# Optimization experiments

Hardware: AMD Instinct MI355X
Metric: run time of the kernel (lower is better)

The kernel has to match this reference:

```python
import jax, jax.numpy as jnp
import numpy as np

C = 512        # concept_num
D = 256        # input_dim / embedding_dim
H = 512        # msg_hidden_dim
M = 256        # msg_output_dim
OH = 512       # hidden_dim
T = 2          # edge_type_num
E = C * (C - 1)  # fully-connected graph without self-loops = 261632


def _glorot(key, shape, fan_in):
    return jax.random.normal(key, shape, jnp.float32) / np.sqrt(fan_in).astype(np.float32)


def setup_inputs() -> dict:
    key = jax.random.key(0)
    ks = jax.random.split(key, 12)
    inputs = jax.random.normal(ks[0], (C, D), jnp.float32)
    rel_type = jax.random.uniform(ks[1], (E, T), jnp.float32)
    send_idx = jax.random.randint(ks[2], (E,), 0, C, jnp.int32)
    rec_idx = jax.random.randint(ks[3], (E,), 0, C, jnp.int32)
    # per-edge-type message MLP params, stacked over type dim
    W1 = _glorot(ks[4], (T, 2 * D, H), 2 * D)
    b1 = jnp.zeros((T, H), jnp.float32)
    W2 = _glorot(ks[5], (T, H, M), H)
    b2 = jnp.zeros((T, M), jnp.float32)
    # output MLP params
    Wo1 = _glorot(ks[6], (M, OH), M)
    bo1 = jnp.zeros((OH,), jnp.float32)
    Wo2 = _glorot(ks[7], (OH, OH), OH)
    bo2 = jnp.zeros((OH,), jnp.float32)
    Wo3 = _glorot(ks[8], (OH, D), OH)
    bo3 = jnp.zeros((D,), jnp.float32)
    return {"inputs": inputs, "rel_type": rel_type, "W1": W1, "b1": b1,
            "W2": W2, "b2": b2, "Wo1": Wo1, "bo1": bo1, "Wo2": Wo2,
            "bo2": bo2, "Wo3": Wo3, "bo3": bo3,
            "send_idx": send_idx, "rec_idx": rec_idx}


def reference(inputs, rel_type, W1, b1, W2, b2, Wo1, bo1, Wo2, bo2, Wo3, bo3,
              send_idx, rec_idx):
    # node2edge: one-hot sparse matmul == index gather
    senders = jnp.take(inputs, send_idx, axis=0)      # [E, D]
    receivers = jnp.take(inputs, rec_idx, axis=0)     # [E, D]
    pre_msg = jnp.concatenate([senders, receivers], axis=-1)  # [E, 2D]
    # per-edge-type MLPs, weighted-summed by rel_type (dropout=0 / eval mode)
    all_msgs = jnp.zeros((pre_msg.shape[0], M), jnp.float32)
    for i in range(T):
        msg = jax.nn.relu(pre_msg @ W1[i] + b1[i])    # [E, H]
        msg = jax.nn.relu(msg @ W2[i] + b2[i])        # [E, M]
        all_msgs = all_msgs + msg * rel_type[:, i:i + 1]
    # edge2node: transposed one-hot sparse matmul == scatter-add over receivers
    agg_msgs = jax.ops.segment_sum(all_msgs, rec_idx, num_segments=inputs.shape[0])  # [C, M]
    pred = jax.nn.relu(agg_msgs @ Wo1 + bo1)
    pred = jax.nn.relu(pred @ Wo2 + bo2)
    return pred @ Wo3 + bo3                           # [C, D]
```

## Files before the change

kernel.cpp:

```cpp
#include <hip/hip_runtime.h>

#define C_N   512
#define E_N   261632
#define CAP   768

typedef _Float16 f16;
typedef _Float16 f16x8_t __attribute__((ext_vector_type(8)));
typedef float    f32x16_t __attribute__((ext_vector_type(16)));

__global__ __launch_bounds__(256) void k_prep_all(
    const float* __restrict__ inputs, const float* __restrict__ W1,
    const float* __restrict__ b1, const float* __restrict__ W2,
    const float* __restrict__ Wo1, const float* __restrict__ Wo2, const float* __restrict__ Wo3,
    f16* __restrict__ SA, f16* __restrict__ RB, f16* __restrict__ W2p,
    f16* __restrict__ Wo1p, f16* __restrict__ Wo2p, f16* __restrict__ Wo3p,
    int* __restrict__ cnt, float* __restrict__ agg)
{
  __shared__ f16 wt[2][256][18];
  int bid = blockIdx.x;
  int tid = threadIdx.x;
  if (bid < 64) {
    int lane = tid & 63, w = tid >> 6;
    int hlf = lane >> 5, l31 = lane & 31;
    int br = bid & 7, bc = (bid >> 3) & 1, mi = bid >> 4;
    int t = mi >> 1, half = mi & 1;
    const float* Wsrc = W1 + (size_t)t * 512 * 512 + (size_t)half * 256 * 512;

    f32x16_t acc[2][2];
    #pragma unroll
    for (int rt = 0; rt < 2; rt++)
      #pragma unroll
      for (int ctl = 0; ctl < 2; ctl++)
        #pragma unroll
        for (int r = 0; r < 16; r++) acc[rt][ctl][r] = 0.f;

    #pragma unroll
    for (int i = 0; i < 4; i++) {
      int idx = tid + i * 256;
      int k = idx >> 6, n4 = idx & 63;
      float4 v = *(const float4*)&Wsrc[(size_t)k * 512 + bc * 256 + n4 * 4];
      wt[0][n4 * 4 + 0][k] = (f16)v.x;
      wt[0][n4 * 4 + 1][k] = (f16)v.y;
      wt[0][n4 * 4 + 2][k] = (f16)v.z;
      wt[0][n4 * 4 + 3][k] = (f16)v.w;
    }

    for (int kc = 0; kc < 16; kc++) {
      __syncthreads();
      if (kc + 1 < 16) {
        int b = (kc + 1) & 1;
        #pragma unroll
        for (int i = 0; i < 4; i++) {
          int idx = tid + i * 256;
          int k = idx >> 6, n4 = idx & 63;
          float4 v = *(const float4*)&Wsrc[(size_t)((kc + 1) * 16 + k) * 512 + bc * 256 + n4 * 4];
          wt[b][n4 * 4 + 0][k] = (f16)v.x;
          wt[b][n4 * 4 + 1][k] = (f16)v.y;
          wt[b][n4 * 4 + 2][k] = (f16)v.z;
          wt[b][n4 * 4 + 3][k] = (f16)v.w;
        }
      }
      f16x8_t af[2];
      #pragma unroll
      for (int rt = 0; rt < 2; rt++) {
        const float4* p = (const float4*)&inputs[(size_t)(br * 64 + rt * 32 + l31) * 256 + kc * 16 + hlf * 8];
        float4 u0 = p[0], u1 = p[1];
        af[rt] = (f16x8_t){(f16)u0.x, (f16)u0.y, (f16)u0.z, (f16)u0.w,
                           (f16)u1.x, (f16)u1.y, (f16)u1.z, (f16)u1.w};
      }
      int b = kc & 1;
      #pragma unroll
      for (int ctl = 0; ctl < 2; ctl++) {
        int n = (2 * w + ctl) * 32 + l31;
        f16x8_t bfr = *(const f16x8_t*)&wt[b][n][hlf * 8];
        #pragma unroll
        for (int rt = 0; rt < 2; rt++)
          acc[rt][ctl] = __builtin_amdgcn_mfma_f32_32x32x16_f16(af[rt], bfr, acc[rt][ctl], 0, 0, 0);
      }
    }
    f16* dst = (half == 0) ? SA : RB;
    #pragma unroll
    for (int ctl = 0; ctl < 2; ctl++) {
      int col = bc * 256 + (2 * w + ctl) * 32 + l31;
      float bias = (half == 1) ? b1[t * 512 + col] : 0.f;
      #pragma unroll
      for (int rt = 0; rt < 2; rt++)
        #pragma unroll
        for (int r = 0; r < 16; r++) {
          int row = br * 64 + rt * 32 + (r & 3) + 8 * (r >> 2) + 4 * hlf;
          dst[((size_t)(t * 512 + row)) * 512 + col] = (f16)(acc[rt][ctl][r] + bias);
        }
    }
  } else if (bid < 192) {
    int gid  = (bid - 64) * 256 + tid;
    int lane = gid & 63;
    int ct   = (gid >> 6) & 7;
    int kc   = (gid >> 9) & 31;
    int t    = gid >> 14;
    int n    = ct * 32 + (lane & 31);
    int k0   = kc * 16 + (lane >> 5) * 8;
    const float* src = W2 + (size_t)t * 512 * 256;
    f16x8_t v;
    #pragma unroll
    for (int j = 0; j < 8; j++) v[j] = (f16)src[(size_t)(k0 + j) * 256 + n];
    *(f16x8_t*)(W2p + (size_t)gid * 8) = v;
  } else if (bid < 256) {
    int gid  = (bid - 192) * 256 + tid;
    int lane = gid & 63;
    int ct   = (gid >> 6) & 15;
    int kc   = gid >> 10;
    int n    = ct * 32 + (lane & 31);
    int k0   = kc * 16 + (lane >> 5) * 8;
    f16x8_t v;
    #pragma unroll
    for (int j = 0; j < 8; j++) v[j] = (f16)Wo1[(size_t)(k0 + j) * 512 + n];
    *(f16x8_t*)(Wo1p + (size_t)gid * 8) = v;
  } else if (bid < 384) {
    int gid  = (bid - 256) * 256 + tid;
    int lane = gid & 63;
    int ct   = (gid >> 6) & 15;
    int kc   = gid >> 10;
    int n    = ct * 32 + (lane & 31);
    int k0   = kc * 16 + (lane >> 5) * 8;
    f16x8_t v;
    #pragma unroll
    for (int j = 0; j < 8; j++) v[j] = (f16)Wo2[(size_t)(k0 + j) * 512 + n];
    *(f16x8_t*)(Wo2p + (size_t)gid * 8) = v;
  } else if (bid < 448) {
    int gid  = (bid - 384) * 256 + tid;
    int lane = gid & 63;
    int ct   = (gid >> 6) & 7;
    int kc   = gid >> 9;
    int n    = ct * 32 + (lane & 31);
    int k0   = kc * 16 + (lane >> 5) * 8;
    f16x8_t v;
    #pragma unroll
    for (int j = 0; j < 8; j++) v[j] = (f16)Wo3[(size_t)(k0 + j) * 256 + n];
    *(f16x8_t*)(Wo3p + (size_t)gid * 8) = v;
  } else if (bid == 448) {
    for (int i = tid; i < 512 * 16; i += 256) cnt[i] = 0;
  } else {
    float4* a4 = (float4*)agg;
    for (int i = tid; i < 512 * 64; i += 256) a4[i] = make_float4(0.f, 0.f, 0.f, 0.f);
  }
}

__global__ __launch_bounds__(512) void k_scatter_d(const int* __restrict__ rec,
    const int* __restrict__ send, const float* __restrict__ rel,
    int* __restrict__ cnt, uint2* __restrict__ smeta)
{
  __shared__ int lh[512];
  __shared__ int lb[512];
  int b = blockIdx.x;
  int e0 = b * (E_N / 128);
  lh[threadIdx.x] = 0;
  __syncthreads();
  for (int i = threadIdx.x; i < E_N / 128; i += 512)
    atomicAdd(&lh[rec[e0 + i]], 1);
  __syncthreads();
  {
    int c = lh[threadIdx.x];
    lb[threadIdx.x] = c ? atomicAdd(&cnt[threadIdx.x * 16], c) : 0;
    lh[threadIdx.x] = 0;
  }
  __syncthreads();
  for (int i = threadIdx.x; i < E_N / 128; i += 512) {
    int e = e0 + i;
    int r = rec[e];
    int p = r * CAP + lb[r] + atomicAdd(&lh[r], 1);
    f16 r0 = (f16)rel[2 * (size_t)e];
    f16 r1 = (f16)rel[2 * (size_t)e + 1];
    unsigned pk = ((unsigned)__builtin_bit_cast(unsigned short, r1) << 16)
                |  (unsigned)__builtin_bit_cast(unsigned short, r0);
    smeta[p] = make_uint2((unsigned)send[e], pk);
  }
}

#define H1S 136

__global__ __launch_bounds__(512, 4) void k_edges(
    const f16* __restrict__ SA, const f16* __restrict__ RB,
    const f16* __restrict__ W2p, const float* __restrict__ b2,
    const uint2* __restrict__ smeta, const int* __restrict__ cnt,
    float* __restrict__ agg)
{
  __shared__ f16   h1[2][128][H1S];
  __shared__ f16   rbs[2][512];
  __shared__ float b2s[2][256];
  __shared__ float aggL[2][256];
  __shared__ __align__(16) float relv[2][128];
  __shared__ int   sends[128];

  int c   = blockIdx.x;
  int ti  = blockIdx.y;
  int n_c = cnt[c * 16];
  if (ti * 128 >= n_c) return;

  int tid  = threadIdx.x;
  int lane = tid & 63;
  int w    = tid >> 6;
  int hlf  = lane >> 5;
  int l31  = lane & 31;
  int q4   = tid & 15;
  int rb0  = tid >> 4;
  int rg   = w >> 2;
  int cg   = w & 3;

  if (tid < 128) {
    int t = tid >> 6, qq = tid & 63;
    *(f16x8_t*)&rbs[t][qq * 8] = *(const f16x8_t*)&RB[((size_t)(t * 512 + c)) * 512 + qq * 8];
  }
  ((float*)aggL)[tid] = 0.f;
  { int t = (tid >> 8) & 1, col = tid & 255; b2s[t][col] = b2[t * 256 + col]; }

  int s0 = c * CAP + ti * 128;
  int nv = n_c - ti * 128; if (nv > 128) nv = 128;

  if (tid < 128) {
    if (tid < nv) {
      uint2 m = smeta[s0 + tid];
      sends[tid] = (int)m.x;
      relv[0][tid] = (float)__builtin_bit_cast(f16, (unsigned short)(m.y & 0xffffu));
      relv[1][tid] = (float)__builtin_bit_cast(f16, (unsigned short)(m.y >> 16));
    } else {
      sends[tid] = 0; relv[0][tid] = 0.f; relv[1][tid] = 0.f;
    }
  }
  __syncthreads();

  const f16x8_t* SAc = (const f16x8_t*)SA;
  const f16x8_t* Bp  = (const f16x8_t*)W2p;

  const f16 fz = (f16)0.f;
  const f16x8_t z8 = {fz, fz, fz, fz, fz, fz, fz, fz};

  int voff[4];
  #pragma unroll
  for (int j = 0; j < 4; j++)
    voff[j] = sends[rb0 + 32 * j] * 64 + q4;

  f16x8_t g[4];

  #pragma unroll
  for (int j = 0; j < 4; j++) g[j] = SAc[voff[j]];
  {
    f16x8_t rbq = *(const f16x8_t*)&rbs[0][q4 * 8];
    #pragma unroll
    for (int j = 0; j < 4; j++) {
      f16x8_t sv = g[j] + rbq;
      sv = __builtin_elementwise_max(sv, z8);
      *(f16x8_t*)&h1[0][rb0 + 32 * j][q4 * 8] = sv;
    }
  }

  f32x16_t acc[2][2];

  for (int p = 0; p < 8; p++) {
    int t  = p >> 2;
    int ks = p & 3;
    int pb = p & 1;
    __syncthreads();

    if (p < 7) {
      int off = ((p + 1) >> 2) * 32768 + ((p + 1) & 3) * 16;
      #pragma unroll
      for (int j = 0; j < 4; j++) g[j] = SAc[voff[j] + off];
    }

    if (ks == 0) {
      #pragma unroll
      for (int a = 0; a < 2; a++)
        #pragma unroll
        for (int b_ = 0; b_ < 2; b_++)
          #pragma unroll
          for (int r = 0; r < 16; r++) acc[a][b_][r] = 0.f;
    }

    const f16x8_t* Bw = Bp + ((size_t)((t * 32 + ks * 8) * 8 + cg * 2) * 64 + lane);

    f16x8_t bb[2][2];
    bb[0][0] = Bw[0];    bb[0][1] = Bw[64];
    bb[1][0] = Bw[512];  bb[1][1] = Bw[512 + 64];

    const f16* h1b = &h1[pb][0][0];
    int a0 = (rg * 64 + l31) * H1S + hlf * 8;
    #pragma unroll
    for (int kc = 0; kc < 8; kc++) {
      int qb = kc & 1;
      f16x8_t af0 = *(const f16x8_t*)&h1b[a0 + kc * 16];
      f16x8_t af1 = *(const f16x8_t*)&h1b[a0 + 32 * H1S + kc * 16];
      acc[0][0] = __builtin_amdgcn_mfma_f32_32x32x16_f16(af0, bb[qb][0], acc[0][0], 0, 0, 0);
      acc[0][1] = __builtin_amdgcn_mfma_f32_32x32x16_f16(af0, bb[qb][1], acc[0][1], 0, 0, 0);
      acc[1][0] = __builtin_amdgcn_mfma_f32_32x32x16_f16(af1, bb[qb][0], acc[1][0], 0, 0, 0);
      acc[1][1] = __builtin_amdgcn_mfma_f32_32x32x16_f16(af1, bb[qb][1], acc[1][1], 0, 0, 0);
      if (kc + 2 < 8) {
        bb[qb][0] = Bw[(kc + 2) * 512];
        bb[qb][1] = Bw[(kc + 2) * 512 + 64];
      }
    }

    if (ks == 3) {
      #pragma unroll
      for (int ctl = 0; ctl < 2; ctl++) {
        int col = (cg * 2 + ctl) * 32 + l31;
        float b2c = b2s[t][col];
        float csum = 0.f;
        #pragma unroll
        for (int rt = 0; rt < 2; rt++) {
          int rbase = rg * 64 + rt * 32 + 4 * hlf;
          #pragma unroll
          for (int grp = 0; grp < 4; grp++) {
            float4 rv = *(const float4*)&relv[t][rbase + 8 * grp];
            float v0 = fmaxf(acc[rt][ctl][grp * 4 + 0] + b2c, 0.f);
            float v1 = fmaxf(acc[rt][ctl][grp * 4 + 1] + b2c, 0.f);
            float v2 = fmaxf(acc[rt][ctl][grp * 4 + 2] + b2c, 0.f);
            float v3 = fmaxf(acc[rt][ctl][grp * 4 + 3] + b2c, 0.f);
            csum += v0 * rv.x + v1 * rv.y + v2 * rv.z + v3 * rv.w;
          }
        }
        csum += __shfl_xor(csum, 32, 64);
        if (hlf == 0) aggL[rg][col] += csum;
      }
    }

    if (p < 7) {
      int tn = (p + 1) >> 2, ksn = (p + 1) & 3;
      f16x8_t rbq = *(const f16x8_t*)&rbs[tn][ksn * 128 + q4 * 8];
      #pragma unroll
      for (int j = 0; j < 4; j++) {
        f16x8_t sv = g[j] + rbq;
        sv = __builtin_elementwise_max(sv, z8);
        *(f16x8_t*)&h1[pb ^ 1][rb0 + 32 * j][q4 * 8] = sv;
      }
    }
  }

  __syncthreads();

  if (tid < 256) atomicAdd(&agg[(size_t)c * 256 + tid], aggL[0][tid] + aggL[1][tid]);
}

#define HOS 520

__global__ __launch_bounds__(512, 1) void k_omlp(const float* __restrict__ agg,
    const f16* __restrict__ Wo1p, const float* __restrict__ bo1,
    const f16* __restrict__ Wo2p, const float* __restrict__ bo2,
    const f16* __restrict__ Wo3p, const float* __restrict__ bo3,
    float* __restrict__ out)
{
  __shared__ f16 hL1[32 * HOS];
  __shared__ f16 hL2[32 * HOS];
  int tid = threadIdx.x, lane = tid & 63, w = tid >> 6;
  int hlf = lane >> 5, l31 = lane & 31;
  int br = blockIdx.x;

  {
    f32x16_t acc[2];
    #pragma unroll
    for (int ctl = 0; ctl < 2; ctl++)
      #pragma unroll
      for (int r = 0; r < 16; r++) acc[ctl][r] = 0.f;
    for (int kc = 0; kc < 16; kc++) {
      const float4* p = (const float4*)&agg[(size_t)(br * 32 + l31) * 256 + kc * 16 + hlf * 8];
      float4 u0 = p[0], u1 = p[1];
      f16x8_t af = (f16x8_t){(f16)u0.x, (f16)u0.y, (f16)u0.z, (f16)u0.w,
                             (f16)u1.x, (f16)u1.y, (f16)u1.z, (f16)u1.w};
      #pragma unroll
      for (int ctl = 0; ctl < 2; ctl++) {
        int ct = 2 * w + ctl;
        f16x8_t bfr = *(const f16x8_t*)&Wo1p[((size_t)(kc * 16 + ct) * 64 + lane) * 8];
        acc[ctl] = __builtin_amdgcn_mfma_f32_32x32x16_f16(af, bfr, acc[ctl], 0, 0, 0);
      }
    }
    #pragma unroll
    for (int ctl = 0; ctl < 2; ctl++) {
      int col = (2 * w + ctl) * 32 + l31;
      float bias = bo1[col];
      #pragma unroll
      for (int r = 0; r < 16; r++) {
        int row = (r & 3) + 8 * (r >> 2) + 4 * hlf;
        hL1[row * HOS + col] = (f16)fmaxf(acc[ctl][r] + bias, 0.f);
      }
    }
  }
  __syncthreads();

  {
    f32x16_t acc[2];
    #pragma unroll
    for (int ctl = 0; ctl < 2; ctl++)
      #pragma unroll
      for (int r = 0; r < 16; r++) acc[ctl][r] = 0.f;
    for (int kc = 0; kc < 32; kc++) {
      f16x8_t af = *(const f16x8_t*)&hL1[l31 * HOS + kc * 16 + hlf * 8];
      #pragma unroll
      for (int ctl = 0; ctl < 2; ctl++) {
        int ct = 2 * w + ctl;
        f16x8_t bfr = *(const f16x8_t*)&Wo2p[((size_t)(kc * 16 + ct) * 64 + lane) * 8];
        acc[ctl] = __builtin_amdgcn_mfma_f32_32x32x16_f16(af, bfr, acc[ctl], 0, 0, 0);
      }
    }
    #pragma unroll
    for (int ctl = 0; ctl < 2; ctl++) {
      int col = (2 * w + ctl) * 32 + l31;
      float bias = bo2[col];
      #pragma unroll
      for (int r = 0; r < 16; r++) {
        int row = (r & 3) + 8 * (r >> 2) + 4 * hlf;
        hL2[row * HOS + col] = (f16)fmaxf(acc[ctl][r] + bias, 0.f);
      }
    }
  }
  __syncthreads();

  {
    f32x16_t acc;
    #pragma unroll
    for (int r = 0; r < 16; r++) acc[r] = 0.f;
    for (int kc = 0; kc < 32; kc++) {
      f16x8_t af  = *(const f16x8_t*)&hL2[l31 * HOS + kc * 16 + hlf * 8];
      f16x8_t bfr = *(const f16x8_t*)&Wo3p[((size_t)(kc * 8 + w) * 64 + lane) * 8];
      acc = __builtin_amdgcn_mfma_f32_32x32x16_f16(af, bfr, acc, 0, 0, 0);
    }
    int col = w * 32 + l31;
    float bias = bo3[col];
    #pragma unroll
    for (int r = 0; r < 16; r++) {
      int row = br * 32 + (r & 3) + 8 * (r >> 2) + 4 * hlf;
      out[(size_t)row * 256 + col] = acc[r] + bias;
    }
  }
}

extern "C" void kernel_launch(void* const* d_in, const int* in_sizes, int n_in,
                              void* d_out, int out_size, void* d_ws, size_t ws_size,
                              hipStream_t stream)
{
  (void)in_sizes; (void)n_in; (void)out_size; (void)ws_size;
  const float* inputs = (const float*)d_in[0];
  const float* rel    = (const float*)d_in[1];
  const float* W1     = (const float*)d_in[2];
  const float* b1     = (const float*)d_in[3];
  const float* W2     = (const float*)d_in[4];
  const float* b2     = (const float*)d_in[5];
  const float* Wo1    = (const float*)d_in[6];
  const float* bo1    = (const float*)d_in[7];
  const float* Wo2    = (const float*)d_in[8];
  const float* bo2    = (const float*)d_in[9];
  const float* Wo3    = (const float*)d_in[10];
  const float* bo3    = (const float*)d_in[11];
  const int* send_idx = (const int*)d_in[12];
  const int* rec_idx  = (const int*)d_in[13];
  float* out = (float*)d_out;

  char* ws = (char*)d_ws;
  f16*    SA    = (f16*)   (ws);
  f16*    RB    = (f16*)   (ws + (1024u << 10));
  f16*    W2p   = (f16*)   (ws + (2048u << 10));
  float*  agg   = (float*) (ws + (2560u << 10));
  int*    cnt   = (int*)   (ws + (3072u << 10));
  f16*    Wo1p  = (f16*)   (ws + (3136u << 10));
  f16*    Wo2p  = (f16*)   (ws + (3392u << 10));
  f16*    Wo3p  = (f16*)   (ws + (3904u << 10));
  uint2*  smeta = (uint2*) (ws + (4160u << 10));

  k_prep_all <<<dim3(450),    dim3(256), 0, stream>>>(inputs, W1, b1, W2, Wo1, Wo2, Wo3,
                                                      SA, RB, W2p, Wo1p, Wo2p, Wo3p, cnt, agg);
  k_scatter_d<<<dim3(128),    dim3(512), 0, stream>>>(rec_idx, send_idx, rel, cnt, smeta);
  k_edges    <<<dim3(512, 5), dim3(512), 0, stream>>>(SA, RB, W2p, b2, smeta, cnt, agg);
  k_omlp     <<<dim3(16),     dim3(512), 0, stream>>>(agg, Wo1p, bo1, Wo2p, bo2, Wo3p, bo3, out);
}
```

Measured before the change: 299.4 us.

## Double k_edges block to 1024 threads with one column tile per wave

```diff
diff --git a/kernel.cpp b/kernel.cpp
--- a/kernel.cpp
+++ b/kernel.cpp
@@ -178,7 +178,7 @@
 
 #define H1S 136
 
-__global__ __launch_bounds__(512, 4) void k_edges(
+__global__ __launch_bounds__(1024, 8) void k_edges(
     const f16* __restrict__ SA, const f16* __restrict__ RB,
     const f16* __restrict__ W2p, const float* __restrict__ b2,
     const uint2* __restrict__ smeta, const int* __restrict__ cnt,
@@ -203,14 +203,14 @@
   int l31  = lane & 31;
   int q4   = tid & 15;
   int rb0  = tid >> 4;
-  int rg   = w >> 2;
-  int cg   = w & 3;
+  int rg   = w >> 3;
+  int cg   = w & 7;
 
   if (tid < 128) {
     int t = tid >> 6, qq = tid & 63;
     *(f16x8_t*)&rbs[t][qq * 8] = *(const f16x8_t*)&RB[((size_t)(t * 512 + c)) * 512 + qq * 8];
   }
-  ((float*)aggL)[tid] = 0.f;
+  if (tid < 512) ((float*)aggL)[tid] = 0.f;
   { int t = (tid >> 8) & 1, col = tid & 255; b2s[t][col] = b2[t * 256 + col]; }
 
   int s0 = c * CAP + ti * 128;
@@ -234,26 +234,26 @@
   const f16 fz = (f16)0.f;
   const f16x8_t z8 = {fz, fz, fz, fz, fz, fz, fz, fz};
 
-  int voff[4];
+  int voff[2];
   #pragma unroll
-  for (int j = 0; j < 4; j++)
-    voff[j] = sends[rb0 + 32 * j] * 64 + q4;
-
-  f16x8_t g[4];
+  for (int j = 0; j < 2; j++)
+    voff[j] = sends[rb0 + 64 * j] * 64 + q4;
+
+  f16x8_t g[2];
 
   #pragma unroll
-  for (int j = 0; j < 4; j++) g[j] = SAc[voff[j]];
+  for (int j = 0; j < 2; j++) g[j] = SAc[voff[j]];
   {
     f16x8_t rbq = *(const f16x8_t*)&rbs[0][q4 * 8];
     #pragma unroll
-    for (int j = 0; j < 4; j++) {
+    for (int j = 0; j < 2; j++) {
       f16x8_t sv = g[j] + rbq;
       sv = __builtin_elementwise_max(sv, z8);
-      *(f16x8_t*)&h1[0][rb0 + 32 * j][q4 * 8] = sv;
-    }
-  }
-
-  f32x16_t acc[2][2];
+      *(f16x8_t*)&h1[0][rb0 + 64 * j][q4 * 8] = sv;
+    }
+  }
+
+  f32x16_t acc[2];
 
   for (int p = 0; p < 8; p++) {
     int t  = p >> 2;
@@ -261,26 +261,23 @@
     int pb = p & 1;
     __syncthreads();
 
+    const f16x8_t* Bw = Bp + ((size_t)((t * 32 + ks * 8) * 8 + cg) * 64 + lane);
+    f16x8_t bb[2];
+    bb[0] = Bw[0];
+    bb[1] = Bw[512];
+
     if (p < 7) {
       int off = ((p + 1) >> 2) * 32768 + ((p + 1) & 3) * 16;
       #pragma unroll
-      for (int j = 0; j < 4; j++) g[j] = SAc[voff[j] + off];
+      for (int j = 0; j < 2; j++) g[j] = SAc[voff[j] + off];
     }
 
     if (ks == 0) {
       #pragma unroll
       for (int a = 0; a < 2; a++)
         #pragma unroll
-        for (int b_ = 0; b_ < 2; b_++)
-          #pragma unroll
-          for (int r = 0; r < 16; r++) acc[a][b_][r] = 0.f;
-    }
-
-    const f16x8_t* Bw = Bp + ((size_t)((t * 32 + ks * 8) * 8 + cg * 2) * 64 + lane);
-
-    f16x8_t bb[2][2];
-    bb[0][0] = Bw[0];    bb[0][1] = Bw[64];
-    bb[1][0] = Bw[512];  bb[1][1] = Bw[512 + 64];
+        for (int r = 0; r < 16; r++) acc[a][r] = 0.f;
+    }
 
     const f16* h1b = &h1[pb][0][0];
     int a0 = (rg * 64 + l31) * H1S + hlf * 8;
@@ -289,48 +286,41 @@
       int qb = kc & 1;
       f16x8_t af0 = *(const f16x8_t*)&h1b[a0 + kc * 16];
       f16x8_t af1 = *(const f16x8_t*)&h1b[a0 + 32 * H1S + kc * 16];
-      acc[0][0] = __builtin_amdgcn_mfma_f32_32x32x16_f16(af0, bb[qb][0], acc[0][0], 0, 0, 0);
-      acc[0][1] = __builtin_amdgcn_mfma_f32_32x32x16_f16(af0, bb[qb][1], acc[0][1], 0, 0, 0);
-      acc[1][0] = __builtin_amdgcn_mfma_f32_32x32x16_f16(af1, bb[qb][0], acc[1][0], 0, 0, 0);
-      acc[1][1] = __builtin_amdgcn_mfma_f32_32x32x16_f16(af1, bb[qb][1], acc[1][1], 0, 0, 0);
-      if (kc + 2 < 8) {
-        bb[qb][0] = Bw[(kc + 2) * 512];
-        bb[qb][1] = Bw[(kc + 2) * 512 + 64];
-      }
+      acc[0] = __builtin_amdgcn_mfma_f32_32x32x16_f16(af0, bb[qb], acc[0], 0, 0, 0);
+      acc[1] = __builtin_amdgcn_mfma_f32_32x32x16_f16(af1, bb[qb], acc[1], 0, 0, 0);
+      if (kc + 2 < 8)
+        bb[qb] = Bw[(kc + 2) * 512];
     }
 
     if (ks == 3) {
-      #pragma unroll
-      for (int ctl = 0; ctl < 2; ctl++) {
-        int col = (cg * 2 + ctl) * 32 + l31;
-        float b2c = b2s[t][col];
-        float csum = 0.f;
-        #pragma unroll
-        for (int rt = 0; rt < 2; rt++) {
-          int rbase = rg * 64 + rt * 32 + 4 * hlf;
-          #pragma unroll
-          for (int grp = 0; grp < 4; grp++) {
-            float4 rv = *(const float4*)&relv[t][rbase + 8 * grp];
-            float v0 = fmaxf(acc[rt][ctl][grp * 4 + 0] + b2c, 0.f);
-            float v1 = fmaxf(acc[rt][ctl][grp * 4 + 1] + b2c, 0.f);
-            float v2 = fmaxf(acc[rt][ctl][grp * 4 + 2] + b2c, 0.f);
-            float v3 = fmaxf(acc[rt][ctl][grp * 4 + 3] + b2c, 0.f);
-            csum += v0 * rv.x + v1 * rv.y + v2 * rv.z + v3 * rv.w;
-          }
+      int col = cg * 32 + l31;
+      float b2c = b2s[t][col];
+      float csum = 0.f;
+      #pragma unroll
+      for (int rt = 0; rt < 2; rt++) {
+        int rbase = rg * 64 + rt * 32 + 4 * hlf;
+        #pragma unroll
+        for (int grp = 0; grp < 4; grp++) {
+          float4 rv = *(const float4*)&relv[t][rbase + 8 * grp];
+          float v0 = fmaxf(acc[rt][grp * 4 + 0] + b2c, 0.f);
+          float v1 = fmaxf(acc[rt][grp * 4 + 1] + b2c, 0.f);
+          float v2 = fmaxf(acc[rt][grp * 4 + 2] + b2c, 0.f);
+          float v3 = fmaxf(acc[rt][grp * 4 + 3] + b2c, 0.f);
+          csum += v0 * rv.x + v1 * rv.y + v2 * rv.z + v3 * rv.w;
         }
-        csum += __shfl_xor(csum, 32, 64);
-        if (hlf == 0) aggL[rg][col] += csum;
-      }
+      }
+      csum += __shfl_xor(csum, 32, 64);
+      if (hlf == 0) aggL[rg][col] += csum;
     }
 
     if (p < 7) {
       int tn = (p + 1) >> 2, ksn = (p + 1) & 3;
       f16x8_t rbq = *(const f16x8_t*)&rbs[tn][ksn * 128 + q4 * 8];
       #pragma unroll
-      for (int j = 0; j < 4; j++) {
+      for (int j = 0; j < 2; j++) {
         f16x8_t sv = g[j] + rbq;
         sv = __builtin_elementwise_max(sv, z8);
-        *(f16x8_t*)&h1[pb ^ 1][rb0 + 32 * j][q4 * 8] = sv;
+        *(f16x8_t*)&h1[pb ^ 1][rb0 + 64 * j][q4 * 8] = sv;
       }
     }
   }
@@ -464,9 +454,9 @@
   f16*    Wo3p  = (f16*)   (ws + (3904u << 10));
   uint2*  smeta = (uint2*) (ws + (4160u << 10));
 
-  k_prep_all <<<dim3(450),    dim3(256), 0, stream>>>(inputs, W1, b1, W2, Wo1, Wo2, Wo3,
-                                                      SA, RB, W2p, Wo1p, Wo2p, Wo3p, cnt, agg);
-  k_scatter_d<<<dim3(128),    dim3(512), 0, stream>>>(rec_idx, send_idx, rel, cnt, smeta);
-  k_edges    <<<dim3(512, 5), dim3(512), 0, stream>>>(SA, RB, W2p, b2, smeta, cnt, agg);
-  k_omlp     <<<dim3(16),     dim3(512), 0, stream>>>(agg, Wo1p, bo1, Wo2p, bo2, Wo3p, bo3, out);
+  k_prep_all <<<dim3(450),    dim3(256),  0, stream>>>(inputs, W1, b1, W2, Wo1, Wo2, Wo3,
+                                                       SA, RB, W2p, Wo1p, Wo2p, Wo3p, cnt, agg);
+  k_scatter_d<<<dim3(128),    dim3(512),  0, stream>>>(rec_idx, send_idx, rel, cnt, smeta);
+  k_edges    <<<dim3(512, 5), dim3(1024), 0, stream>>>(SA, RB, W2p, b2, smeta, cnt, agg);
+  k_omlp     <<<dim3(16),     dim3(512),  0, stream>>>(agg, Wo1p, bo1, Wo2p, bo2, Wo3p, bo3, out);
 }
```

Result: slower. 357.6 us (+19.4%).
